# Performance work log

Measured on AMD Instinct MI355X. Metric: run time of the kernel, lower is better.

The kernel has to match this reference:

```python
import jax, jax.numpy as jnp
import numpy as np

B, T, S, D, H, DK, DV, DFF = 2, 2048, 2048, 1024, 16, 64, 64, 4096
EPS = 1e-5


def layer_norm(x, g, b):
    m = jnp.mean(x, axis=-1, keepdims=True)
    v = jnp.var(x, axis=-1, keepdims=True)
    return (x - m) * jax.lax.rsqrt(v + EPS) * g + b


def mha(q_in, k_in, v_in, Wq, bq, Wk, bk, Wv, bv, Wo, bo, mask):
    # q_in: [B, Lq, D]; k_in/v_in: [B, Lk, D]
    Q = (q_in @ Wq + bq).reshape(q_in.shape[0], -1, H, DK).transpose(0, 2, 1, 3)  # [B,H,Lq,dk]
    K = (k_in @ Wk + bk).reshape(k_in.shape[0], -1, H, DK).transpose(0, 2, 1, 3)
    V = (v_in @ Wv + bv).reshape(v_in.shape[0], -1, H, DV).transpose(0, 2, 1, 3)
    scores = jnp.einsum('bhqd,bhkd->bhqk', Q, K) / jnp.float32(np.sqrt(DK))
    scores = jnp.where(mask == 0, jnp.float32(-1e9), scores)
    attn = jax.nn.softmax(scores, axis=-1)
    out = jnp.einsum('bhqk,bhkd->bhqd', attn, V)
    out = out.transpose(0, 2, 1, 3).reshape(q_in.shape[0], -1, H * DV)
    return out @ Wo + bo


def setup_inputs() -> dict:
    key = jax.random.key(0)
    ks = jax.random.split(key, 16)
    s = 0.02
    inp = {
        'x': jax.random.normal(ks[0], (B, T, D), jnp.float32),
        'encoder_output': jax.random.normal(ks[1], (B, S, D), jnp.float32),
        'lookahead_mask': jnp.tril(jnp.ones((T, T), jnp.int32))[None, None],  # [1,1,T,T]
        'padding_mask': jnp.ones((1, 1, 1, S), jnp.int32),
        # self-attention params
        'sa_Wq': jax.random.normal(ks[2], (D, H * DK), jnp.float32) * s,
        'sa_bq': jnp.zeros((H * DK,), jnp.float32),
        'sa_Wk': jax.random.normal(ks[3], (D, H * DK), jnp.float32) * s,
        'sa_bk': jnp.zeros((H * DK,), jnp.float32),
        'sa_Wv': jax.random.normal(ks[4], (D, H * DV), jnp.float32) * s,
        'sa_bv': jnp.zeros((H * DV,), jnp.float32),
        'sa_Wo': jax.random.normal(ks[5], (H * DV, D), jnp.float32) * s,
        'sa_bo': jnp.zeros((D,), jnp.float32),
        # cross-attention params
        'ca_Wq': jax.random.normal(ks[6], (D, H * DK), jnp.float32) * s,
        'ca_bq': jnp.zeros((H * DK,), jnp.float32),
        'ca_Wk': jax.random.normal(ks[7], (D, H * DK), jnp.float32) * s,
        'ca_bk': jnp.zeros((H * DK,), jnp.float32),
        'ca_Wv': jax.random.normal(ks[8], (D, H * DV), jnp.float32) * s,
        'ca_bv': jnp.zeros((H * DV,), jnp.float32),
        'ca_Wo': jax.random.normal(ks[9], (H * DV, D), jnp.float32) * s,
        'ca_bo': jnp.zeros((D,), jnp.float32),
        # feed-forward params
        'ff_W1': jax.random.normal(ks[10], (D, DFF), jnp.float32) * s,
        'ff_b1': jnp.zeros((DFF,), jnp.float32),
        'ff_W2': jax.random.normal(ks[11], (DFF, D), jnp.float32) * s,
        'ff_b2': jnp.zeros((D,), jnp.float32),
        # layer norms
        'ln1_g': jnp.ones((D,), jnp.float32), 'ln1_b': jnp.zeros((D,), jnp.float32),
        'ln2_g': jnp.ones((D,), jnp.float32), 'ln2_b': jnp.zeros((D,), jnp.float32),
        'ln3_g': jnp.ones((D,), jnp.float32), 'ln3_b': jnp.zeros((D,), jnp.float32),
    }
    return inp


def reference(x, encoder_output, lookahead_mask, padding_mask,
              sa_Wq, sa_bq, sa_Wk, sa_bk, sa_Wv, sa_bv, sa_Wo, sa_bo,
              ca_Wq, ca_bq, ca_Wk, ca_bk, ca_Wv, ca_bv, ca_Wo, ca_bo,
              ff_W1, ff_b1, ff_W2, ff_b2,
              ln1_g, ln1_b, ln2_g, ln2_b, ln3_g, ln3_b):
    attn1 = mha(x, x, x, sa_Wq, sa_bq, sa_Wk, sa_bk, sa_Wv, sa_bv, sa_Wo, sa_bo, lookahead_mask)
    addnorm1 = layer_norm(x + attn1, ln1_g, ln1_b)
    attn2 = mha(addnorm1, encoder_output, encoder_output,
                ca_Wq, ca_bq, ca_Wk, ca_bk, ca_Wv, ca_bv, ca_Wo, ca_bo, padding_mask)
    addnorm2 = layer_norm(addnorm1 + attn2, ln2_g, ln2_b)
    ff = jax.nn.relu(addnorm2 @ ff_W1 + ff_b1) @ ff_W2 + ff_b2
    return layer_norm(addnorm2 + ff, ln3_g, ln3_b)
```

## Files before the change

kernel.cpp:

```cpp
#include <hip/hip_runtime.h>

typedef unsigned short u16;
typedef unsigned int   u32;
typedef __attribute__((ext_vector_type(8)))  __bf16 bf16x8;
typedef __attribute__((ext_vector_type(4)))  float  f32x4;
typedef __attribute__((ext_vector_type(16))) float  f32x16;
typedef __attribute__((ext_vector_type(4)))  unsigned short u16x4;

#define DEV static __device__ __forceinline__

#define SC 0.1803368801111243f

DEV u16 cvt_bf16(float f){
  u32 u = __builtin_bit_cast(u32, f);
  u32 r = (u + 0x7FFFu + ((u >> 16) & 1u)) >> 16;
  return (u16)r;
}

typedef __attribute__((address_space(1))) void* as1p;
typedef __attribute__((address_space(3))) void* as3p;

DEV void gld16(void* lds, const void* g){
  __builtin_amdgcn_global_load_lds((as1p)g, (as3p)lds, 16, 0, 0);
}

DEV f32x4 mfma16(bf16x8 a, bf16x8 b, f32x4 c){
  return __builtin_amdgcn_mfma_f32_16x16x32_bf16(a, b, c, 0, 0, 0);
}
DEV f32x16 mfma32(bf16x8 a, bf16x8 b, f32x16 c){
  return __builtin_amdgcn_mfma_f32_32x32x16_bf16(a, b, c, 0, 0, 0);
}

DEV bf16x8 ld8(const u16* p){ return *(const bf16x8*)p; }

DEV float vexp2(float x){
  float y; asm("v_exp_f32 %0, %1" : "=v"(y) : "v"(x)); return y;
}

DEV u32 cvtpk(float lo, float hi){
  u32 r; asm("v_cvt_pk_bf16_f32 %0, %1, %2" : "=v"(r) : "v"(lo), "v"(hi)); return r;
}
DEV void perm32swap(u32 &a, u32 &b){
  asm("v_permlane32_swap_b32 %0, %1" : "+v"(a), "+v"(b));
}
DEV bf16x8 frag4(u32 w0,u32 w1,u32 w2,u32 w3){
  union{ u32 w[4]; bf16x8 f; } u; u.w[0]=w0; u.w[1]=w1; u.w[2]=w2; u.w[3]=w3; return u.f;
}

DEV int swz64(int row, int blk){ return row*64 + ((blk ^ (row & 7)) << 3); }
DEV int swz32(int row, int blk){ return row*32 + ((blk ^ (row & 3)) << 3); }

__global__ __launch_bounds__(256) void castk(const float* __restrict__ in,
                                             u16* __restrict__ out, int n4){
  int i = blockIdx.x*256 + threadIdx.x;
  if(i >= n4) return;
  f32x4 v = *(const f32x4*)(in + (size_t)i*4);
  u16x4 o;
  #pragma unroll
  for(int j=0;j<4;j++) o[j] = cvt_bf16(v[j]);
  *(u16x4*)(out + (size_t)i*4) = o;
}

__global__ __launch_bounds__(256) void fcopy(const float* __restrict__ s,
                                             float* __restrict__ d, int n){
  int i = blockIdx.x*256 + threadIdx.x;
  if(i < n) d[i] = s[i];
}

__global__ __launch_bounds__(256) void maskbias(const int* __restrict__ pm,
                                                float* __restrict__ bias, int n){
  int i = blockIdx.x*256 + threadIdx.x;
  if(i < n) bias[i] = pm[i] ? 0.f : -8e9f;
}

__global__ __launch_bounds__(256) void wcast_t(const float* __restrict__ W,
                                               u16* __restrict__ Wt, int K, int N){
  __shared__ u16 tile[64][66];
  const int k0 = blockIdx.x*64, n0 = blockIdx.y*64;
  const int lr = threadIdx.x >> 4, c4 = (threadIdx.x & 15)*4;
  #pragma unroll
  for(int p=0;p<4;p++){
    const int r = lr + p*16;
    f32x4 v = *(const f32x4*)&W[(size_t)(k0+r)*N + n0 + c4];
    #pragma unroll
    for(int j=0;j<4;j++) tile[r][c4+j] = cvt_bf16(v[j]);
  }
  __syncthreads();
  #pragma unroll
  for(int p=0;p<4;p++){
    const int n = lr + p*16;
    u16x4 u;
    #pragma unroll
    for(int j=0;j<4;j++) u[j] = tile[c4+j][n];
    *(u16x4*)&Wt[(size_t)(n0+n)*K + k0 + c4] = u;
  }
}

__global__ __launch_bounds__(256) void vtrans(const u16* __restrict__ V,
                                              u16* __restrict__ Vt, int L, int ld){
  __shared__ u16 tile[64][66];
  const int t0 = blockIdx.x*64;
  const int h = blockIdx.y, b = blockIdx.z;
  const int lr = threadIdx.x >> 4, c4 = (threadIdx.x & 15)*4;
  #pragma unroll
  for(int p=0;p<4;p++){
    const int r = lr + p*16;
    u16x4 v = *(const u16x4*)&V[(size_t)(b*L + t0 + r)*ld + h*64 + c4];
    #pragma unroll
    for(int j=0;j<4;j++) tile[r][c4+j] = v[j];
  }
  __syncthreads();
  #pragma unroll
  for(int p=0;p<4;p++){
    const int d = lr + p*16;
    u16x4 u;
    #pragma unroll
    for(int j=0;j<4;j++) u[j] = tile[c4+j][d];
    *(u16x4*)&Vt[((size_t)((b*16 + h)*64 + d))*L + t0 + c4] = u;
  }
}

template<int OMODE, int BN>
__global__ __launch_bounds__(256, BN==128 ? 3 : 4) void gemm_bt(
    const u16* __restrict__ A, const u16* __restrict__ Bt,
    const float* __restrict__ bias, void* __restrict__ Cout,
    int N, int K)
{
  __shared__ __align__(16) u16 As[2][128*32];
  __shared__ __align__(16) u16 Bs[2][BN*32];
  constexpr int NJ = BN/32;
  const int tid = threadIdx.x, wave = tid>>6, lane = tid&63;
  const int fr = lane&15, fg = lane>>4;
  const int bm = blockIdx.x*128, bn = blockIdx.y*BN;
  const int wm = (wave>>1)*64, wn = (wave&1)*(BN/2);
  const f32x4 z4 = {0.f,0.f,0.f,0.f};
  f32x4 acc[4][NJ];
  #pragma unroll
  for(int i=0;i<4;i++)
    #pragma unroll
    for(int j=0;j<NJ;j++) acc[i][j] = z4;

  const int srA = wave*32 + (lane>>2);
  const int cl_l = (lane&3)*8;
  const int cl_g = ((lane&3) ^ ((lane>>2)&3))*8;
  const int srB = (BN==128) ? srA : (wave*16 + (lane>>2));
  const u16* gA = A  + (size_t)(bm + srA)*K + cl_g;
  const u16* gB = Bt + (size_t)(bn + srB)*K + cl_g;

  auto stage = [&](int p, int ko){
    u16* lA = &As[p][srA*32 + cl_l];
    u16* lB = &Bs[p][srB*32 + cl_l];
    gld16(lA,     gA + ko);
    gld16(lA+512, gA + ko + (size_t)16*K);
    gld16(lB,     gB + ko);
    if(BN==128) gld16(lB+512, gB + ko + (size_t)16*K);
  };

  const int nk = K >> 5;
  stage(0, 0);
  __syncthreads();
  for(int kt=0; kt<nk; ++kt){
    const int cur = kt & 1;
    if(kt+1 < nk) stage(cur^1, (kt+1)*32);
    bf16x8 af[4], bfv[NJ];
    #pragma unroll
    for(int i=0;i<4;i++) af[i] = ld8(&As[cur][swz32(wm + i*16 + fr, fg)]);
    #pragma unroll
    for(int j=0;j<NJ;j++) bfv[j] = ld8(&Bs[cur][swz32(wn + j*16 + fr, fg)]);
    __builtin_amdgcn_s_setprio(1);
    #pragma unroll
    for(int i=0;i<4;i++)
      #pragma unroll
      for(int j=0;j<NJ;j++)
        acc[i][j] = mfma16(af[i], bfv[j], acc[i][j]);
    __builtin_amdgcn_s_setprio(0);
    __syncthreads();
  }

  const int r0 = bm + wm + fg*4;
  const int c0 = bn + wn + fr;
  #pragma unroll
  for(int j=0;j<NJ;j++){
    const int col = c0 + j*16;
    const float bv = bias[col];
    #pragma unroll
    for(int i=0;i<4;i++){
      #pragma unroll
      for(int r=0;r<4;r++){
        const float v = acc[i][j][r] + bv;
        const size_t idx = (size_t)(r0 + i*16 + r)*N + col;
        if(OMODE==0)      ((float*)Cout)[idx] = v;
        else if(OMODE==1) ((u16*)Cout)[idx]   = cvt_bf16(v);
        else              ((u16*)Cout)[idx]   = cvt_bf16(fmaxf(v, 0.f));
      }
    }
  }
}

template<bool CAUSAL>
__global__ __launch_bounds__(256,4) void attn3(
    const u16* __restrict__ Qg, int ldq, const u16* __restrict__ Kg, int ldk,
    const u16* __restrict__ Vt, const float* __restrict__ biasg,
    float* __restrict__ Opart, float* __restrict__ Ml, float* __restrict__ Ll,
    int Lk)
{
  __shared__ __align__(16) u16 Ks[2][64*64];
  __shared__ __align__(16) u16 Vs[2][64*64];
  __shared__ float FacL[4][32];
  const int tid = threadIdx.x, wave = tid>>6, lane = tid&63;
  const int l31 = lane&31, hi = lane>>5;
  const int bid = blockIdx.x;
  const int g    = (bid&7)*4 + (bid>>8);
  const int r5   = (bid>>3)&31;
  const int part = r5&1, qb = r5>>1;
  const int h = g&15, b = g>>4;
  const int qi = CAUSAL ? ((qb&1) ? (15-(qb>>1)) : (qb>>1)) : qb;
  const int q0 = qi*128;
  const int qw = q0 + wave*32;
  const int qrow = qw + l31;

  bf16x8 qf[4];
  {
    const u16* Qp = Qg + (size_t)(b*2048 + qrow)*ldq + h*64;
    #pragma unroll
    for(int c=0;c<4;c++) qf[c] = ld8(Qp + c*16 + hi*8);
  }

  f32x16 o0, o1;
  #pragma unroll
  for(int r=0;r<16;r++){ o0[r]=0.f; o1[r]=0.f; }
  float m = -3e38f, lsum = 0.f;

  const int srow = wave*16 + (lane>>3);
  const int cl_l = (lane&7)*8;
  const int cl_g = ((lane&7) ^ ((lane>>3)&7))*8;
  const u16* Kp = Kg + (size_t)(b*2048 + srow)*ldk + h*64 + cl_g;
  const u16* Vp = Vt + ((size_t)((b*16 + h)*64 + srow))*Lk + cl_g;

  auto stage = [&](int p, int kv0){
    u16* lK = &Ks[p][srow*64 + cl_l];
    u16* lV = &Vs[p][srow*64 + cl_l];
    gld16(lK,     Kp + (size_t)kv0*ldk);
    gld16(lK+512, Kp + (size_t)(kv0+8)*ldk);
    gld16(lV,     Vp + kv0);
    gld16(lV+512, Vp + kv0 + 8*(size_t)Lk);
  };

  const int span = CAUSAL ? (qi+1) : ((Lk>>6)>>1);
  const int t0 = part*span, t1 = t0 + span;

  stage(0, t0*64);
  __syncthreads();
  for(int kt=t0; kt<t1; ++kt){
    const int cur = (kt-t0)&1;
    const int kv0 = kt*64;
    if(kt+1 < t1) stage(cur^1, (kt+1)*64);

    if(!CAUSAL || kv0 <= qw+31){
      f32x16 s0, s1;
      #pragma unroll
      for(int r=0;r<16;r++){ s0[r]=0.f; s1[r]=0.f; }
      __builtin_amdgcn_s_setprio(1);
      #pragma unroll
      for(int c=0;c<4;c++){
        bf16x8 k0 = ld8(&Ks[cur][swz64(l31,      2*c+hi)]);
        bf16x8 k1 = ld8(&Ks[cur][swz64(32 + l31, 2*c+hi)]);
        s0 = mfma32(k0, qf[c], s0);
        s1 = mfma32(k1, qf[c], s1);
      }
      __builtin_amdgcn_s_setprio(0);

      float p[32];
      #pragma unroll
      for(int r=0;r<16;r++){ p[r]=s0[r]; p[16+r]=s1[r]; }

      if(CAUSAL){
        if(kv0 + 63 > qw){
          #pragma unroll
          for(int n=0;n<2;n++)
            #pragma unroll
            for(int r=0;r<16;r++){
              const int kc = kv0 + 32*n + (r&3) + 8*(r>>2) + 4*hi;
              if(kc > qrow) p[16*n+r] = -8e9f;
            }
        }
      } else {
        #pragma unroll
        for(int n=0;n<2;n++)
          #pragma unroll
          for(int cq=0;cq<4;cq++){
            f32x4 bv = *(const f32x4*)&biasg[kv0 + 32*n + 8*cq + 4*hi];
            #pragma unroll
            for(int i=0;i<4;i++) p[16*n+4*cq+i] += bv[i];
          }
      }

      float pm = p[0];
      #pragma unroll
      for(int r=1;r<32;r++) pm = fmaxf(pm, p[r]);
      pm = fmaxf(pm, __shfl_xor(pm, 32));
      if(__any(pm > m + 64.f)){
        const float nm = fmaxf(m, pm);
        const float fac = vexp2((m - nm)*SC);
        lsum *= fac;
        FacL[wave][l31] = fac;
        #pragma unroll
        for(int r=0;r<16;r++){
          const int qidx = (r&3) + 8*(r>>2) + 4*hi;
          const float fb = FacL[wave][qidx];
          o0[r] *= fb; o1[r] *= fb;
        }
        m = nm;
      }
      float rs = 0.f;
      #pragma unroll
      for(int r=0;r<32;r++){ p[r] = vexp2((p[r]-m)*SC); rs += p[r]; }
      rs += __shfl_xor(rs, 32);
      lsum += rs;

      u32 pw[16];
      #pragma unroll
      for(int n=0;n<2;n++)
        #pragma unroll
        for(int cp=0;cp<2;cp++){
          const int base = 16*n + 8*cp, cc = 2*n + cp;
          u32 a1 = cvtpk(p[base+0], p[base+1]);
          u32 a2 = cvtpk(p[base+2], p[base+3]);
          u32 b1 = cvtpk(p[base+4], p[base+5]);
          u32 b2 = cvtpk(p[base+6], p[base+7]);
          perm32swap(a1, b1);
          perm32swap(a2, b2);
          pw[4*cc+0]=a1; pw[4*cc+1]=a2; pw[4*cc+2]=b1; pw[4*cc+3]=b2;
        }

      __builtin_amdgcn_s_setprio(1);
      #pragma unroll
      for(int cc=0;cc<4;cc++){
        bf16x8 pf = frag4(pw[4*cc], pw[4*cc+1], pw[4*cc+2], pw[4*cc+3]);
        bf16x8 v0 = ld8(&Vs[cur][swz64(l31,      2*cc+hi)]);
        bf16x8 v1 = ld8(&Vs[cur][swz64(32 + l31, 2*cc+hi)]);
        o0 = mfma32(pf, v0, o0);
        o1 = mfma32(pf, v1, o1);
      }
      __builtin_amdgcn_s_setprio(0);
    }
    __syncthreads();
  }

  float* Op = Opart + (size_t)part*4194304 + (size_t)(b*2048 + qw)*1024 + h*64;
  #pragma unroll
  for(int r=0;r<16;r++){
    const int qidx = (r&3) + 8*(r>>2) + 4*hi;
    Op[(size_t)qidx*1024 + l31]      = o0[r];
    Op[(size_t)qidx*1024 + 32 + l31] = o1[r];
  }
  if(hi==0){
    const int mi = part*65536 + (b*2048 + qw + l31)*16 + h;
    Ml[mi] = m; Ll[mi] = lsum;
  }
}

__global__ __launch_bounds__(256) void att_combine(
    const float* __restrict__ O0, const float* __restrict__ O1,
    const float* __restrict__ Ml, const float* __restrict__ Ll,
    u16* __restrict__ Ob)
{
  const int row = blockIdx.x, tid = threadIdx.x;
  const int h = tid>>4;
  const int mi = row*16 + h;
  const float m0 = Ml[mi], m1 = Ml[65536+mi];
  const float l0 = Ll[mi], l1 = Ll[65536+mi];
  const float mx = fmaxf(m0, m1);
  const float w0 = vexp2((m0-mx)*SC), w1 = vexp2((m1-mx)*SC);
  const float inv = 1.f/(w0*l0 + w1*l1);
  const size_t base = (size_t)row*1024 + tid*4;
  f32x4 a = *(const f32x4*)(O0 + base);
  f32x4 c = *(const f32x4*)(O1 + base);
  u16x4 o;
  #pragma unroll
  for(int j=0;j<4;j++) o[j] = cvt_bf16((w0*a[j] + w1*c[j])*inv);
  *(u16x4*)(Ob + base) = o;
}

__global__ __launch_bounds__(256) void add_ln(const float* __restrict__ X,
                        const float* __restrict__ Dl,
                        const float* __restrict__ gam, const float* __restrict__ bet,
                        float* __restrict__ outf, u16* __restrict__ outb){
  __shared__ float red[8];
  const int tid = threadIdx.x, wave = tid>>6, lane = tid&63;
  const size_t base = ((size_t)blockIdx.x << 10) + tid*4;
  f32x4 xv = *(const f32x4*)(X + base);
  f32x4 dv = *(const f32x4*)(Dl + base);
  f32x4 v;
  #pragma unroll
  for(int j=0;j<4;j++) v[j] = xv[j] + dv[j];
  float s = v[0]+v[1]+v[2]+v[3];
  float q = v[0]*v[0]+v[1]*v[1]+v[2]*v[2]+v[3]*v[3];
  #pragma unroll
  for(int off=1;off<64;off<<=1){ s += __shfl_xor(s,off); q += __shfl_xor(q,off); }
  if(lane==0){ red[wave]=s; red[4+wave]=q; }
  __syncthreads();
  s = red[0]+red[1]+red[2]+red[3];
  q = red[4]+red[5]+red[6]+red[7];
  const float mean = s*(1.f/1024.f);
  const float var  = q*(1.f/1024.f) - mean*mean;
  const float rr = rsqrtf(var + 1e-5f);
  const int c = tid*4;
  f32x4 y;
  #pragma unroll
  for(int j=0;j<4;j++) y[j] = (v[j]-mean)*rr*gam[c+j] + bet[c+j];
  *(f32x4*)(outf + base) = y;
  if(outb){
    u16x4 ob;
    #pragma unroll
    for(int j=0;j<4;j++) ob[j] = cvt_bf16(y[j]);
    *(u16x4*)(outb + base) = ob;
  }
}

extern "C" void kernel_launch(void* const* d_in, const int* in_sizes, int n_in,
                              void* d_out, int out_size, void* d_ws, size_t ws_size,
                              hipStream_t stream)
{
  (void)in_sizes; (void)n_in; (void)out_size; (void)ws_size;
  const float* x    = (const float*)d_in[0];
  const float* enc  = (const float*)d_in[1];
  const int*   pmask= (const int*)d_in[3];
  const float* saWq = (const float*)d_in[4];  const float* sabq = (const float*)d_in[5];
  const float* saWk = (const float*)d_in[6];  const float* sabk = (const float*)d_in[7];
  const float* saWv = (const float*)d_in[8];  const float* sabv = (const float*)d_in[9];
  const float* saWo = (const float*)d_in[10]; const float* sabo = (const float*)d_in[11];
  const float* caWq = (const float*)d_in[12]; const float* cabq = (const float*)d_in[13];
  const float* caWk = (const float*)d_in[14]; const float* cabk = (const float*)d_in[15];
  const float* caWv = (const float*)d_in[16]; const float* cabv = (const float*)d_in[17];
  const float* caWo = (const float*)d_in[18]; const float* cabo = (const float*)d_in[19];
  const float* fW1  = (const float*)d_in[20]; const float* fb1  = (const float*)d_in[21];
  const float* fW2  = (const float*)d_in[22]; const float* fb2  = (const float*)d_in[23];
  const float* l1g  = (const float*)d_in[24]; const float* l1b  = (const float*)d_in[25];
  const float* l2g  = (const float*)d_in[26]; const float* l2b  = (const float*)d_in[27];
  const float* l3g  = (const float*)d_in[28]; const float* l3b  = (const float*)d_in[29];

  char* wsp = (char*)d_ws;
  size_t off = 0;
  auto take = [&](size_t bytes)->void*{ void* p = wsp + off; off += (bytes + 255) & ~(size_t)255; return p; };
  u16* slotA  = (u16*)take(8388608);
  u16* Encb   = (u16*)take(8388608);
  u16* WqkvT  = (u16*)take(6291456);
  u16* cWqT   = (u16*)take(2097152);
  u16* cWkvT  = (u16*)take(4194304);
  u16* WoT    = (u16*)take(2097152);
  u16* cWoT   = (u16*)take(2097152);
  u16* W1T    = (u16*)take(8388608);
  u16* W2T    = (u16*)take(8388608);
  float* bqkv = (float*)take(16384);
  float* bkvc = (float*)take(16384);
  float* biasg= (float*)take(16384);
  u16* slotB  = (u16*)take(25165824);
  u16* Vtb    = (u16*)take(8388608);
  u16* Ob     = (u16*)take(8388608);
  u16* an1b   = (u16*)take(8388608);
  float* projf= (float*)take(16777216);
  float* an1f = (float*)take(16777216);
  float* an2f = (float*)take(16777216);
  char* ffhb  = (char*)take(33554432);
  u16* Xbf = slotA;  u16* Qcb = slotA;  u16* an2b = slotA;
  u16* QKVb = slotB; u16* KVc = slotB;
  u16* ffh   = (u16*)ffhb;
  float* Opar = (float*)ffhb;
  float* Mlb = (float*)an1b;
  float* Llb = Mlb + 131072;

  castk<<<4096,256,0,stream>>>(x,   Xbf,  1048576);
  castk<<<4096,256,0,stream>>>(enc, Encb, 1048576);
  wcast_t<<<dim3(16,16),256,0,stream>>>(saWq, WqkvT,                1024, 1024);
  wcast_t<<<dim3(16,16),256,0,stream>>>(saWk, WqkvT + 1024*1024,    1024, 1024);
  wcast_t<<<dim3(16,16),256,0,stream>>>(saWv, WqkvT + 2*1024*1024,  1024, 1024);
  wcast_t<<<dim3(16,16),256,0,stream>>>(saWo, WoT, 1024, 1024);
  wcast_t<<<dim3(16,16),256,0,stream>>>(caWq, cWqT, 1024, 1024);
  wcast_t<<<dim3(16,16),256,0,stream>>>(caWk, cWkvT,               1024, 1024);
  wcast_t<<<dim3(16,16),256,0,stream>>>(caWv, cWkvT + 1024*1024,   1024, 1024);
  wcast_t<<<dim3(16,16),256,0,stream>>>(caWo, cWoT, 1024, 1024);
  wcast_t<<<dim3(16,64),256,0,stream>>>(fW1, W1T, 1024, 4096);
  wcast_t<<<dim3(64,16),256,0,stream>>>(fW2, W2T, 4096, 1024);
  fcopy<<<4,256,0,stream>>>(sabq, bqkv,        1024);
  fcopy<<<4,256,0,stream>>>(sabk, bqkv + 1024, 1024);
  fcopy<<<4,256,0,stream>>>(sabv, bqkv + 2048, 1024);
  fcopy<<<4,256,0,stream>>>(cabk, bkvc,        1024);
  fcopy<<<4,256,0,stream>>>(cabv, bkvc + 1024, 1024);
  maskbias<<<8,256,0,stream>>>(pmask, biasg, 2048);

  gemm_bt<1,128><<<dim3(32,24),256,0,stream>>>(Xbf, WqkvT, bqkv, QKVb, 3072, 1024);
  vtrans<<<dim3(32,16,2),256,0,stream>>>(QKVb + 2048, Vtb, 2048, 3072);
  attn3<true><<<1024,256,0,stream>>>(QKVb, 3072, QKVb + 1024, 3072, Vtb, nullptr,
                                     Opar, Mlb, Llb, 2048);
  att_combine<<<4096,256,0,stream>>>(Opar, Opar + 4194304, Mlb, Llb, Ob);
  gemm_bt<0,64><<<dim3(32,16),256,0,stream>>>(Ob, WoT, sabo, projf, 1024, 1024);
  add_ln<<<4096,256,0,stream>>>(x, projf, l1g, l1b, an1f, an1b);

  gemm_bt<1,64><<<dim3(32,16),256,0,stream>>>(an1b, cWqT, cabq, Qcb, 1024, 1024);
  gemm_bt<1,128><<<dim3(32,16),256,0,stream>>>(Encb, cWkvT, bkvc, KVc, 2048, 1024);
  vtrans<<<dim3(32,16,2),256,0,stream>>>(KVc + 1024, Vtb, 2048, 2048);
  attn3<false><<<1024,256,0,stream>>>(Qcb, 1024, KVc, 2048, Vtb, biasg,
                                      Opar, Mlb, Llb, 2048);
  att_combine<<<4096,256,0,stream>>>(Opar, Opar + 4194304, Mlb, Llb, Ob);
  gemm_bt<0,64><<<dim3(32,16),256,0,stream>>>(Ob, cWoT, cabo, projf, 1024, 1024);
  add_ln<<<4096,256,0,stream>>>(an1f, projf, l2g, l2b, an2f, an2b);

  gemm_bt<2,128><<<dim3(32,32),256,0,stream>>>(an2b, W1T, fb1, ffh, 4096, 1024);
  gemm_bt<0,64><<<dim3(32,16),256,0,stream>>>(ffh, W2T, fb2, projf, 1024, 4096);
  add_ln<<<4096,256,0,stream>>>(an2f, projf, l3g, l3b, (float*)d_out, nullptr);
}
```

Before: 454.2 us.

## Split-K output-projection GEMMs into wider tiles and fuse partial sums into LayerNorm

The three N=1024 output GEMMs (two attention output projections and FFN down-projection) move from 128x64 tiles to 128x128 tiles with a 2-way K split. This keeps the block count at 512 while improving operand reuse per block. The second partial is written to a spare fp32 buffer and summed inside a new add_ln3 kernel, which adds extra global traffic for the partial tensors. Separately, the weight-cast, input-cast, bias-copy and mask kernels are merged into a few multi-tensor launches to cut launch overhead.

```diff
diff --git a/kernel.cpp b/kernel.cpp
--- a/kernel.cpp
+++ b/kernel.cpp
@@ -50,10 +50,13 @@
 DEV int swz64(int row, int blk){ return row*64 + ((blk ^ (row & 7)) << 3); }
 DEV int swz32(int row, int blk){ return row*32 + ((blk ^ (row & 3)) << 3); }
 
-__global__ __launch_bounds__(256) void castk(const float* __restrict__ in,
-                                             u16* __restrict__ out, int n4){
+__global__ __launch_bounds__(256) void castk2(const float* __restrict__ in0,
+                                              u16* __restrict__ out0,
+                                              const float* __restrict__ in1,
+                                              u16* __restrict__ out1){
+  const float* in = blockIdx.y ? in1 : in0;
+  u16*        out = blockIdx.y ? out1 : out0;
   int i = blockIdx.x*256 + threadIdx.x;
-  if(i >= n4) return;
   f32x4 v = *(const f32x4*)(in + (size_t)i*4);
   u16x4 o;
   #pragma unroll
@@ -61,23 +64,25 @@
   *(u16x4*)(out + (size_t)i*4) = o;
 }
 
-__global__ __launch_bounds__(256) void fcopy(const float* __restrict__ s,
-                                             float* __restrict__ d, int n){
+__global__ __launch_bounds__(256) void smallfuse(
+    const float* __restrict__ sabq, const float* __restrict__ sabk,
+    const float* __restrict__ sabv, const float* __restrict__ cabk,
+    const float* __restrict__ cabv, const int* __restrict__ pm,
+    float* __restrict__ bqkv, float* __restrict__ bkvc, float* __restrict__ biasg){
   int i = blockIdx.x*256 + threadIdx.x;
-  if(i < n) d[i] = s[i];
-}
-
-__global__ __launch_bounds__(256) void maskbias(const int* __restrict__ pm,
-                                                float* __restrict__ bias, int n){
-  int i = blockIdx.x*256 + threadIdx.x;
-  if(i < n) bias[i] = pm[i] ? 0.f : -8e9f;
-}
-
-__global__ __launch_bounds__(256) void wcast_t(const float* __restrict__ W,
-                                               u16* __restrict__ Wt, int K, int N){
+  if(i < 1024)       bqkv[i] = sabq[i];
+  else if(i < 2048)  bqkv[i] = sabk[i-1024];
+  else if(i < 3072)  bqkv[i] = sabv[i-2048];
+  else if(i < 4096)  bkvc[i-3072] = cabk[i-3072];
+  else if(i < 5120)  bkvc[i-3072] = cabv[i-4096];
+  else if(i < 7168)  biasg[i-5120] = pm[i-5120] ? 0.f : -8e9f;
+}
+
+DEV void wcast_body(const float* __restrict__ W, u16* __restrict__ Wt,
+                    int K, int N, int bx, int by, int tid){
   __shared__ u16 tile[64][66];
-  const int k0 = blockIdx.x*64, n0 = blockIdx.y*64;
-  const int lr = threadIdx.x >> 4, c4 = (threadIdx.x & 15)*4;
+  const int k0 = bx*64, n0 = by*64;
+  const int lr = tid >> 4, c4 = (tid & 15)*4;
   #pragma unroll
   for(int p=0;p<4;p++){
     const int r = lr + p*16;
@@ -94,6 +99,25 @@
     for(int j=0;j<4;j++) u[j] = tile[c4+j][n];
     *(u16x4*)&Wt[(size_t)(n0+n)*K + k0 + c4] = u;
   }
+}
+
+__global__ __launch_bounds__(256) void wcast_t(const float* __restrict__ W,
+                                               u16* __restrict__ Wt, int K, int N){
+  wcast_body(W, Wt, K, N, blockIdx.x, blockIdx.y, threadIdx.x);
+}
+
+__global__ __launch_bounds__(256) void wcast8(
+    const float* s0, const float* s1, const float* s2, const float* s3,
+    const float* s4, const float* s5, const float* s6, const float* s7,
+    u16* d0, u16* d1, u16* d2, u16* d3, u16* d4, u16* d5, u16* d6, u16* d7){
+  const float* W; u16* Wt;
+  switch(blockIdx.z){
+    case 0: W=s0; Wt=d0; break;  case 1: W=s1; Wt=d1; break;
+    case 2: W=s2; Wt=d2; break;  case 3: W=s3; Wt=d3; break;
+    case 4: W=s4; Wt=d4; break;  case 5: W=s5; Wt=d5; break;
+    case 6: W=s6; Wt=d6; break;  default: W=s7; Wt=d7; break;
+  }
+  wcast_body(W, Wt, 1024, 1024, blockIdx.x, blockIdx.y, threadIdx.x);
 }
 
 __global__ __launch_bounds__(256) void vtrans(const u16* __restrict__ V,
@@ -120,10 +144,10 @@
   }
 }
 
-template<int OMODE, int BN>
+template<int OMODE, int BN, int SPLITK>
 __global__ __launch_bounds__(256, BN==128 ? 3 : 4) void gemm_bt(
     const u16* __restrict__ A, const u16* __restrict__ Bt,
-    const float* __restrict__ bias, void* __restrict__ Cout,
+    const float* __restrict__ bias, void* __restrict__ Cout0, void* __restrict__ Cout1,
     int N, int K)
 {
   __shared__ __align__(16) u16 As[2][128*32];
@@ -132,6 +156,9 @@
   const int tid = threadIdx.x, wave = tid>>6, lane = tid&63;
   const int fr = lane&15, fg = lane>>4;
   const int bm = blockIdx.x*128, bn = blockIdx.y*BN;
+  const int part = (SPLITK>1) ? blockIdx.z : 0;
+  const int Kp = K / SPLITK;
+  const int kbase = part * Kp;
   const int wm = (wave>>1)*64, wn = (wave&1)*(BN/2);
   const f32x4 z4 = {0.f,0.f,0.f,0.f};
   f32x4 acc[4][NJ];
@@ -144,8 +171,8 @@
   const int cl_l = (lane&3)*8;
   const int cl_g = ((lane&3) ^ ((lane>>2)&3))*8;
   const int srB = (BN==128) ? srA : (wave*16 + (lane>>2));
-  const u16* gA = A  + (size_t)(bm + srA)*K + cl_g;
-  const u16* gB = Bt + (size_t)(bn + srB)*K + cl_g;
+  const u16* gA = A  + (size_t)(bm + srA)*K + kbase + cl_g;
+  const u16* gB = Bt + (size_t)(bn + srB)*K + kbase + cl_g;
 
   auto stage = [&](int p, int ko){
     u16* lA = &As[p][srA*32 + cl_l];
@@ -156,7 +183,7 @@
     if(BN==128) gld16(lB+512, gB + ko + (size_t)16*K);
   };
 
-  const int nk = K >> 5;
+  const int nk = Kp >> 5;
   stage(0, 0);
   __syncthreads();
   for(int kt=0; kt<nk; ++kt){
@@ -177,12 +204,13 @@
     __syncthreads();
   }
 
+  void* Cout = (part==0) ? Cout0 : Cout1;
   const int r0 = bm + wm + fg*4;
   const int c0 = bn + wn + fr;
   #pragma unroll
   for(int j=0;j<NJ;j++){
     const int col = c0 + j*16;
-    const float bv = bias[col];
+    const float bv = (part==0) ? bias[col] : 0.f;
     #pragma unroll
     for(int i=0;i<4;i++){
       #pragma unroll
@@ -382,18 +410,19 @@
   *(u16x4*)(Ob + base) = o;
 }
 
-__global__ __launch_bounds__(256) void add_ln(const float* __restrict__ X,
-                        const float* __restrict__ Dl,
+__global__ __launch_bounds__(256) void add_ln3(const float* __restrict__ X,
+                        const float* __restrict__ D1, const float* __restrict__ D2,
                         const float* __restrict__ gam, const float* __restrict__ bet,
                         float* __restrict__ outf, u16* __restrict__ outb){
   __shared__ float red[8];
   const int tid = threadIdx.x, wave = tid>>6, lane = tid&63;
   const size_t base = ((size_t)blockIdx.x << 10) + tid*4;
   f32x4 xv = *(const f32x4*)(X + base);
-  f32x4 dv = *(const f32x4*)(Dl + base);
+  f32x4 d1 = *(const f32x4*)(D1 + base);
+  f32x4 d2 = *(const f32x4*)(D2 + base);
   f32x4 v;
   #pragma unroll
-  for(int j=0;j<4;j++) v[j] = xv[j] + dv[j];
+  for(int j=0;j<4;j++) v[j] = xv[j] + d1[j] + d2[j];
   float s = v[0]+v[1]+v[2]+v[3];
   float q = v[0]*v[0]+v[1]*v[1]+v[2]*v[2]+v[3]*v[3];
   #pragma unroll
@@ -470,43 +499,34 @@
   float* Mlb = (float*)an1b;
   float* Llb = Mlb + 131072;
 
-  castk<<<4096,256,0,stream>>>(x,   Xbf,  1048576);
-  castk<<<4096,256,0,stream>>>(enc, Encb, 1048576);
-  wcast_t<<<dim3(16,16),256,0,stream>>>(saWq, WqkvT,                1024, 1024);
-  wcast_t<<<dim3(16,16),256,0,stream>>>(saWk, WqkvT + 1024*1024,    1024, 1024);
-  wcast_t<<<dim3(16,16),256,0,stream>>>(saWv, WqkvT + 2*1024*1024,  1024, 1024);
-  wcast_t<<<dim3(16,16),256,0,stream>>>(saWo, WoT, 1024, 1024);
-  wcast_t<<<dim3(16,16),256,0,stream>>>(caWq, cWqT, 1024, 1024);
-  wcast_t<<<dim3(16,16),256,0,stream>>>(caWk, cWkvT,               1024, 1024);
-  wcast_t<<<dim3(16,16),256,0,stream>>>(caWv, cWkvT + 1024*1024,   1024, 1024);
-  wcast_t<<<dim3(16,16),256,0,stream>>>(caWo, cWoT, 1024, 1024);
+  castk2<<<dim3(4096,2),256,0,stream>>>(x, Xbf, enc, Encb);
+  wcast8<<<dim3(16,16,8),256,0,stream>>>(
+      saWq, saWk, saWv, saWo, caWq, caWk, caWv, caWo,
+      WqkvT, WqkvT + 1024*1024, WqkvT + 2*1024*1024, WoT,
+      cWqT, cWkvT, cWkvT + 1024*1024, cWoT);
   wcast_t<<<dim3(16,64),256,0,stream>>>(fW1, W1T, 1024, 4096);
   wcast_t<<<dim3(64,16),256,0,stream>>>(fW2, W2T, 4096, 1024);
-  fcopy<<<4,256,0,stream>>>(sabq, bqkv,        1024);
-  fcopy<<<4,256,0,stream>>>(sabk, bqkv + 1024, 1024);
-  fcopy<<<4,256,0,stream>>>(sabv, bqkv + 2048, 1024);
-  fcopy<<<4,256,0,stream>>>(cabk, bkvc,        1024);
-  fcopy<<<4,256,0,stream>>>(cabv, bkvc + 1024, 1024);
-  maskbias<<<8,256,0,stream>>>(pmask, biasg, 2048);
-
-  gemm_bt<1,128><<<dim3(32,24),256,0,stream>>>(Xbf, WqkvT, bqkv, QKVb, 3072, 1024);
+  smallfuse<<<28,256,0,stream>>>(sabq, sabk, sabv, cabk, cabv, pmask,
+                                 bqkv, bkvc, biasg);
+
+  gemm_bt<1,128,1><<<dim3(32,24),256,0,stream>>>(Xbf, WqkvT, bqkv, QKVb, nullptr, 3072, 1024);
   vtrans<<<dim3(32,16,2),256,0,stream>>>(QKVb + 2048, Vtb, 2048, 3072);
   attn3<true><<<1024,256,0,stream>>>(QKVb, 3072, QKVb + 1024, 3072, Vtb, nullptr,
                                      Opar, Mlb, Llb, 2048);
   att_combine<<<4096,256,0,stream>>>(Opar, Opar + 4194304, Mlb, Llb, Ob);
-  gemm_bt<0,64><<<dim3(32,16),256,0,stream>>>(Ob, WoT, sabo, projf, 1024, 1024);
-  add_ln<<<4096,256,0,stream>>>(x, projf, l1g, l1b, an1f, an1b);
-
-  gemm_bt<1,64><<<dim3(32,16),256,0,stream>>>(an1b, cWqT, cabq, Qcb, 1024, 1024);
-  gemm_bt<1,128><<<dim3(32,16),256,0,stream>>>(Encb, cWkvT, bkvc, KVc, 2048, 1024);
+  gemm_bt<0,128,2><<<dim3(32,8,2),256,0,stream>>>(Ob, WoT, sabo, projf, an2f, 1024, 1024);
+  add_ln3<<<4096,256,0,stream>>>(x, projf, an2f, l1g, l1b, an1f, an1b);
+
+  gemm_bt<1,64,1><<<dim3(32,16),256,0,stream>>>(an1b, cWqT, cabq, Qcb, nullptr, 1024, 1024);
+  gemm_bt<1,128,1><<<dim3(32,16),256,0,stream>>>(Encb, cWkvT, bkvc, KVc, nullptr, 2048, 1024);
   vtrans<<<dim3(32,16,2),256,0,stream>>>(KVc + 1024, Vtb, 2048, 2048);
   attn3<false><<<1024,256,0,stream>>>(Qcb, 1024, KVc, 2048, Vtb, biasg,
                                       Opar, Mlb, Llb, 2048);
   att_combine<<<4096,256,0,stream>>>(Opar, Opar + 4194304, Mlb, Llb, Ob);
-  gemm_bt<0,64><<<dim3(32,16),256,0,stream>>>(Ob, cWoT, cabo, projf, 1024, 1024);
-  add_ln<<<4096,256,0,stream>>>(an1f, projf, l2g, l2b, an2f, an2b);
-
-  gemm_bt<2,128><<<dim3(32,32),256,0,stream>>>(an2b, W1T, fb1, ffh, 4096, 1024);
-  gemm_bt<0,64><<<dim3(32,16),256,0,stream>>>(ffh, W2T, fb2, projf, 1024, 4096);
-  add_ln<<<4096,256,0,stream>>>(an2f, projf, l3g, l3b, (float*)d_out, nullptr);
-}
+  gemm_bt<0,128,2><<<dim3(32,8,2),256,0,stream>>>(Ob, cWoT, cabo, projf, Opar, 1024, 1024);
+  add_ln3<<<4096,256,0,stream>>>(an1f, projf, Opar, l2g, l2b, an2f, an2b);
+
+  gemm_bt<2,128,1><<<dim3(32,32),256,0,stream>>>(an2b, W1T, fb1, ffh, nullptr, 4096, 1024);
+  gemm_bt<0,128,2><<<dim3(32,8,2),256,0,stream>>>(ffh, W2T, fb2, projf, an1f, 1024, 4096);
+  add_ln3<<<4096,256,0,stream>>>(an2f, projf, an1f, l3g, l3b, (float*)d_out, nullptr);
+}
```

Result: faster. 422.8 us (-6.9%).
